# Kernel tuning notes

Hardware: AMD Instinct MI355X
Metric: run time of the kernel (lower is better)

Reference implementation:

```python
import jax, jax.numpy as jnp
import numpy as np
import math

BS, S, DIM, H = 2, 2048, 1024, 16
DH = DIM // H


def setup_inputs() -> dict:
    key = jax.random.key(0)
    ks = jax.random.split(key, 11)
    std = 1.0 / math.sqrt(DIM)
    inp = {
        "query": jax.random.normal(ks[0], (BS, S, DIM), jnp.float32),
        "key_": jax.random.normal(ks[1], (BS, S, DIM), jnp.float32),
        "value": jax.random.normal(ks[2], (BS, S, DIM), jnp.float32),
        "mask": jnp.ones((BS, S), jnp.int32),
        "q_w": jax.random.normal(ks[3], (DIM, DIM), jnp.float32) * std,
        "q_b": jnp.zeros((DIM,), jnp.float32),
        "k_w": jax.random.normal(ks[4], (DIM, DIM), jnp.float32) * std,
        "k_b": jnp.zeros((DIM,), jnp.float32),
        "v_w": jax.random.normal(ks[5], (DIM, DIM), jnp.float32) * std,
        "v_b": jnp.zeros((DIM,), jnp.float32),
        "o_w": jax.random.normal(ks[6], (DIM, DIM), jnp.float32) * std,
        "o_b": jnp.zeros((DIM,), jnp.float32),
    }
    return inp


def _shape(x):
    # (bs, s, dim) -> (bs, h, s, dh)
    return x.reshape(BS, -1, H, DH).transpose(0, 2, 1, 3)


def reference(query, key_, value, mask, q_w, q_b, k_w, k_b, v_w, v_b, o_w, o_b):
    # linear projections (torch Linear: x @ W.T + b)
    q = _shape(query @ q_w.T + q_b) / math.sqrt(DH)
    k = _shape(key_ @ k_w.T + k_b)
    v = _shape(value @ v_w.T + v_b)
    # scores: (bs, h, s, s)
    scores = jnp.einsum("bhqd,bhkd->bhqk", q, k)
    pad = (mask == 0)[:, None, None, :]  # (bs,1,1,k_len)
    scores = jnp.where(pad, -jnp.inf, scores)
    weights = jax.nn.softmax(scores, axis=-1)
    context = jnp.einsum("bhqk,bhkd->bhqd", weights, v)
    context = context.transpose(0, 2, 1, 3).reshape(BS, -1, DIM)
    return context @ o_w.T + o_b
```

## Files before the change

kernel.cpp:

```cpp
#include <hip/hip_runtime.h>
#include <hip/hip_bf16.h>

#define BSZ 2
#define SEQ 2048
#define DIMN 1024
#define NH 16
#define DH 64
#define LOG2E 1.4426950408889634f

typedef unsigned short ushort_t;
typedef __attribute__((ext_vector_type(8))) short short8;
typedef __attribute__((ext_vector_type(4))) float float4v;

__device__ __forceinline__ ushort_t f2bf(float f) {
    union { float f; unsigned int u; } c; c.f = f;
    return (ushort_t)((c.u + 0x8000u) >> 16);
}
__device__ __forceinline__ unsigned int pkbf(float a, float b) {
    __hip_bfloat162 h = __float22bfloat162_rn(make_float2(a, b));
    unsigned int u; __builtin_memcpy(&u, &h, 4); return u;
}
__device__ __forceinline__ unsigned int pkbf_asm(float a, float b) {
    unsigned int d;
    asm("v_cvt_pk_bf16_f32 %0, %1, %2" : "=v"(d) : "v"(a), "v"(b));
    return d;
}
__device__ __forceinline__ float exp2_raw(float x) {
    float d; asm("v_exp_f32 %0, %1" : "=v"(d) : "v"(x)); return d;
}
__device__ __forceinline__ float max3f(float a, float b, float c) {
    float d; asm("v_max3_f32 %0, %1, %2, %3" : "=v"(d) : "v"(a), "v"(b), "v"(c)); return d;
}
__device__ __forceinline__ void gld16(const ushort_t* g, ushort_t* l) {
    __builtin_amdgcn_global_load_lds(
        (const __attribute__((address_space(1))) unsigned int*)g,
        (__attribute__((address_space(3))) unsigned int*)l, 16, 0, 0);
}

__global__ __launch_bounds__(256) void cvt_all(
    const float* __restrict__ w0, const float* __restrict__ w1,
    const float* __restrict__ w2, const float* __restrict__ w3,
    const float* __restrict__ x0, const float* __restrict__ x1,
    const float* __restrict__ x2,
    ushort_t* __restrict__ o0, ushort_t* __restrict__ o1,
    ushort_t* __restrict__ o2, ushort_t* __restrict__ o3,
    ushort_t* __restrict__ xb)
{
    const int y = blockIdx.y;
    if (y < 4) {
        const float* s; ushort_t* d;
        switch (y) {
            case 0: s = w0; d = o0; break;
            case 1: s = w1; d = o1; break;
            case 2: s = w2; d = o2; break;
            default: s = w3; d = o3; break;
        }
        int i = (blockIdx.x * 256 + threadIdx.x) * 4;
        float4v v = *(const float4v*)(s + i);
        uint2 o; o.x = pkbf(v[0], v[1]); o.y = pkbf(v[2], v[3]);
        *(uint2*)(d + i) = o;
    } else {
        const int m = y - 4;
        const float* s = (m == 0) ? x0 : (m == 1) ? x1 : x2;
        ushort_t* d = xb + (size_t)m * (BSZ * SEQ * DIMN);
        size_t base = (size_t)blockIdx.x * 4096;
#pragma unroll
        for (int j = 0; j < 4; ++j) {
            size_t i = base + j * 1024 + threadIdx.x * 4;
            float4v v = *(const float4v*)(s + i);
            uint2 o; o.x = pkbf(v[0], v[1]); o.y = pkbf(v[2], v[3]);
            *(uint2*)(d + i) = o;
        }
    }
}

__global__ __launch_bounds__(256) void gemm_qkv(
    const float* __restrict__ xq, const float* __restrict__ xk, const float* __restrict__ xv,
    const ushort_t* __restrict__ Wq, const ushort_t* __restrict__ Wk, const ushort_t* __restrict__ Wv,
    const float* __restrict__ qb, const float* __restrict__ kb, const float* __restrict__ vb,
    ushort_t* __restrict__ Qp, ushort_t* __restrict__ Kp, ushort_t* __restrict__ VpT)
{
    __shared__ ushort_t As[128 * 72];
    __shared__ ushort_t Bs[128 * 72];
    const int tid  = threadIdx.x;
    const int lane = tid & 63;
    const int w    = tid >> 6;
    const int wm   = w >> 1, wn = w & 1;
    const int quad = lane >> 4;
    const int l16  = lane & 15;
    const int mBase = blockIdx.y * 128;
    const int nGlob = blockIdx.x * 128;
    const int z     = nGlob >> 10;
    const int nBase = nGlob & 1023;
    const float*    A    = (z == 0) ? xq : (z == 1) ? xk : xv;
    const ushort_t* W    = (z == 0) ? Wq : (z == 1) ? Wk : Wv;
    const float*    bias = (z == 0) ? qb : (z == 1) ? kb : vb;

    float4v acc[4][4];
    const float4v z4 = {0.f, 0.f, 0.f, 0.f};
#pragma unroll
    for (int i = 0; i < 4; ++i)
#pragma unroll
        for (int j = 0; j < 4; ++j) acc[i][j] = z4;

    for (int k0 = 0; k0 < 1024; k0 += 64) {
        float4v a[4][2];
        short8  wb[4];
#pragma unroll
        for (int it = 0; it < 4; ++it) {
            int c = it * 256 + tid, row = c >> 3, col = (c & 7) * 8;
            const float* g = A + (size_t)(mBase + row) * 1024 + k0 + col;
            a[it][0] = *(const float4v*)g;
            a[it][1] = *(const float4v*)(g + 4);
            wb[it] = *(const short8*)(W + (size_t)(nBase + row) * 1024 + k0 + col);
        }
        __syncthreads();
#pragma unroll
        for (int it = 0; it < 4; ++it) {
            int c = it * 256 + tid, row = c >> 3, col = (c & 7) * 8;
            uint4 ua;
            ua.x = pkbf(a[it][0][0], a[it][0][1]); ua.y = pkbf(a[it][0][2], a[it][0][3]);
            ua.z = pkbf(a[it][1][0], a[it][1][1]); ua.w = pkbf(a[it][1][2], a[it][1][3]);
            *(uint4*)&As[row * 72 + col] = ua;
            *(short8*)&Bs[row * 72 + col] = wb[it];
        }
        __syncthreads();

#pragma unroll
        for (int ksub = 0; ksub < 2; ++ksub) {
            short8 af[4], bf[4];
#pragma unroll
            for (int mt = 0; mt < 4; ++mt)
                af[mt] = *(const short8*)&As[(wm * 64 + mt * 16 + l16) * 72 + ksub * 32 + quad * 8];
#pragma unroll
            for (int nt = 0; nt < 4; ++nt)
                bf[nt] = *(const short8*)&Bs[(wn * 64 + nt * 16 + l16) * 72 + ksub * 32 + quad * 8];
#pragma unroll
            for (int mt = 0; mt < 4; ++mt)
#pragma unroll
                for (int nt = 0; nt < 4; ++nt)
                    acc[mt][nt] = __builtin_amdgcn_mfma_f32_16x16x32_bf16(af[mt], bf[nt], acc[mt][nt], 0, 0, 0);
        }
    }

    const float scale = (z == 0) ? 0.125f * LOG2E : 1.0f;
    if (z < 2) {
        ushort_t* C = (z == 0) ? Qp : Kp;
#pragma unroll
        for (int mt = 0; mt < 4; ++mt)
#pragma unroll
            for (int nt = 0; nt < 4; ++nt) {
                int colg = nBase + wn * 64 + nt * 16 + l16;
                float bv = bias[colg];
#pragma unroll
                for (int r = 0; r < 4; ++r) {
                    int rowg = mBase + wm * 64 + mt * 16 + quad * 4 + r;
                    C[(size_t)rowg * 1024 + colg] = f2bf((acc[mt][nt][r] + bv) * scale);
                }
            }
    } else {
#pragma unroll
        for (int mt = 0; mt < 4; ++mt)
#pragma unroll
            for (int nt = 0; nt < 4; ++nt) {
                int n = nBase + wn * 64 + nt * 16 + l16;
                int hh = n >> 6, d = n & 63;
                float bv = bias[n];
                int rowg = mBase + wm * 64 + mt * 16 + quad * 4;
                int b = rowg >> 11, s = rowg & 2047;
                uint2 pk;
                pk.x = pkbf(acc[mt][nt][0] + bv, acc[mt][nt][1] + bv);
                pk.y = pkbf(acc[mt][nt][2] + bv, acc[mt][nt][3] + bv);
                *(uint2*)&VpT[(((size_t)(b * 16 + hh) * 64 + d) << 11) + s] = pk;
            }
    }
}

__global__ __launch_bounds__(256) void gemm_qkv_fast(
    const ushort_t* __restrict__ Xb,
    const ushort_t* __restrict__ Wq, const ushort_t* __restrict__ Wk, const ushort_t* __restrict__ Wv,
    const float* __restrict__ qb, const float* __restrict__ kb, const float* __restrict__ vb,
    ushort_t* __restrict__ Qp, ushort_t* __restrict__ Kp, ushort_t* __restrict__ VpT)
{
    __shared__ __align__(16) ushort_t As[128 * 64];
    __shared__ __align__(16) ushort_t Bs[128 * 64];
    const int tid  = threadIdx.x;
    const int lane = tid & 63;
    const int w    = tid >> 6;
    const int wm   = w >> 1, wn = w & 1;
    const int quad = lane >> 4;
    const int l16  = lane & 15;
    const int sw   = l16 & 7;
    const int mBase = blockIdx.y * 128;
    const int nGlob = blockIdx.x * 128;
    const int z     = nGlob >> 10;
    const int nBase = nGlob & 1023;
    const ushort_t* A    = Xb + (size_t)z * (BSZ * SEQ * DIMN);
    const ushort_t* W    = (z == 0) ? Wq : (z == 1) ? Wk : Wv;
    const float*    bias = (z == 0) ? qb : (z == 1) ? kb : vb;

    const int srow = tid >> 3;
    const int sc   = tid & 7;

    float4v acc[4][4];
    const float4v z4 = {0.f, 0.f, 0.f, 0.f};
#pragma unroll
    for (int i = 0; i < 4; ++i)
#pragma unroll
        for (int j = 0; j < 4; ++j) acc[i][j] = z4;

    for (int k0 = 0; k0 < 1024; k0 += 64) {
#pragma unroll
        for (int itq = 0; itq < 4; ++itq) {
            int row = itq * 32 + srow;
            int colsw = (sc ^ (row & 7)) * 8;
            gld16(A + (size_t)(mBase + row) * 1024 + k0 + colsw, &As[(itq * 32 + w * 8) * 64]);
            gld16(W + (size_t)(nBase + row) * 1024 + k0 + colsw, &Bs[(itq * 32 + w * 8) * 64]);
        }
        __syncthreads();

#pragma unroll
        for (int ksub = 0; ksub < 2; ++ksub) {
            short8 af[4], bf[4];
#pragma unroll
            for (int mt = 0; mt < 4; ++mt)
                af[mt] = *(const short8*)&As[(wm * 64 + mt * 16 + l16) * 64 + ((ksub * 4 + quad) ^ sw) * 8];
#pragma unroll
            for (int nt = 0; nt < 4; ++nt)
                bf[nt] = *(const short8*)&Bs[(wn * 64 + nt * 16 + l16) * 64 + ((ksub * 4 + quad) ^ sw) * 8];
#pragma unroll
            for (int mt = 0; mt < 4; ++mt)
#pragma unroll
                for (int nt = 0; nt < 4; ++nt)
                    acc[mt][nt] = __builtin_amdgcn_mfma_f32_16x16x32_bf16(af[mt], bf[nt], acc[mt][nt], 0, 0, 0);
        }
        __syncthreads();
    }

    const float scale = (z == 0) ? 0.125f * LOG2E : 1.0f;
    if (z < 2) {
        ushort_t* C = (z == 0) ? Qp : Kp;
#pragma unroll
        for (int mt = 0; mt < 4; ++mt)
#pragma unroll
            for (int nt = 0; nt < 4; ++nt) {
                int colg = nBase + wn * 64 + nt * 16 + l16;
                float bv = bias[colg];
#pragma unroll
                for (int r = 0; r < 4; ++r) {
                    int rowg = mBase + wm * 64 + mt * 16 + quad * 4 + r;
                    C[(size_t)rowg * 1024 + colg] = f2bf((acc[mt][nt][r] + bv) * scale);
                }
            }
    } else {
#pragma unroll
        for (int mt = 0; mt < 4; ++mt)
#pragma unroll
            for (int nt = 0; nt < 4; ++nt) {
                int n = nBase + wn * 64 + nt * 16 + l16;
                int hh = n >> 6, d = n & 63;
                float bv = bias[n];
                int rowg = mBase + wm * 64 + mt * 16 + quad * 4;
                int b = rowg >> 11, s = rowg & 2047;
                uint2 pk;
                pk.x = pkbf(acc[mt][nt][0] + bv, acc[mt][nt][1] + bv);
                pk.y = pkbf(acc[mt][nt][2] + bv, acc[mt][nt][3] + bv);
                *(uint2*)&VpT[(((size_t)(b * 16 + hh) * 64 + d) << 11) + s] = pk;
            }
    }
}

__global__ __launch_bounds__(256) void gemm_o(
    const ushort_t* __restrict__ A, const ushort_t* __restrict__ W,
    const float* __restrict__ bias, float* __restrict__ C)
{
    __shared__ ushort_t As[128 * 72];
    __shared__ ushort_t Bs[64 * 72];
    const int tid  = threadIdx.x;
    const int lane = tid & 63;
    const int w    = tid >> 6;
    const int wm   = w & 1, wn = w >> 1;
    const int quad = lane >> 4;
    const int l16  = lane & 15;
    const int mBase = blockIdx.y * 128;
    const int nBase = blockIdx.x * 64;

    float4v acc[4][2];
    const float4v z4 = {0.f, 0.f, 0.f, 0.f};
#pragma unroll
    for (int mt = 0; mt < 4; ++mt)
#pragma unroll
        for (int nt = 0; nt < 2; ++nt) acc[mt][nt] = z4;

    for (int k0 = 0; k0 < 1024; k0 += 64) {
        short8 ab[4], wb[2];
#pragma unroll
        for (int it = 0; it < 4; ++it) {
            int c = it * 256 + tid, row = c >> 3, col = (c & 7) * 8;
            ab[it] = *(const short8*)(A + (size_t)(mBase + row) * 1024 + k0 + col);
        }
#pragma unroll
        for (int it = 0; it < 2; ++it) {
            int c = it * 256 + tid, row = c >> 3, col = (c & 7) * 8;
            wb[it] = *(const short8*)(W + (size_t)(nBase + row) * 1024 + k0 + col);
        }
        __syncthreads();
#pragma unroll
        for (int it = 0; it < 4; ++it) {
            int c = it * 256 + tid, row = c >> 3, col = (c & 7) * 8;
            *(short8*)&As[row * 72 + col] = ab[it];
        }
#pragma unroll
        for (int it = 0; it < 2; ++it) {
            int c = it * 256 + tid, row = c >> 3, col = (c & 7) * 8;
            *(short8*)&Bs[row * 72 + col] = wb[it];
        }
        __syncthreads();

#pragma unroll
        for (int ksub = 0; ksub < 2; ++ksub) {
            short8 af[4], bf[2];
#pragma unroll
            for (int mt = 0; mt < 4; ++mt)
                af[mt] = *(const short8*)&As[(wm * 64 + mt * 16 + l16) * 72 + ksub * 32 + quad * 8];
#pragma unroll
            for (int nt = 0; nt < 2; ++nt)
                bf[nt] = *(const short8*)&Bs[(wn * 32 + nt * 16 + l16) * 72 + ksub * 32 + quad * 8];
#pragma unroll
            for (int mt = 0; mt < 4; ++mt)
#pragma unroll
                for (int nt = 0; nt < 2; ++nt)
                    acc[mt][nt] = __builtin_amdgcn_mfma_f32_16x16x32_bf16(af[mt], bf[nt], acc[mt][nt], 0, 0, 0);
        }
    }

#pragma unroll
    for (int mt = 0; mt < 4; ++mt)
#pragma unroll
        for (int nt = 0; nt < 2; ++nt) {
            int colg = nBase + wn * 32 + nt * 16 + l16;
            float bv = bias[colg];
#pragma unroll
            for (int r = 0; r < 4; ++r) {
                int rowg = mBase + wm * 64 + mt * 16 + quad * 4 + r;
                C[(size_t)rowg * 1024 + colg] = acc[mt][nt][r] + bv;
            }
        }
}

__global__ __launch_bounds__(512) void attn_kernel(
    const ushort_t* __restrict__ Qp, const ushort_t* __restrict__ Kp,
    const ushort_t* __restrict__ VpT, const int* __restrict__ mask,
    ushort_t* __restrict__ Cp)
{
    __shared__ __align__(16) ushort_t Qs[128 * 64];
    __shared__ __align__(16) ushort_t Ks[2][64 * 64];
    __shared__ __align__(16) ushort_t Vt[2][64 * 64];
    __shared__ int s_mok[8];

    const int tid  = threadIdx.x;
    const int lane = tid & 63;
    const int w    = tid >> 6;
    const int quad = lane >> 4;
    const int l16  = lane & 15;
    const int sw   = l16 & 7;
    const int b    = blockIdx.x >> 4;
    const int h    = blockIdx.x & 15;
    const int q0   = blockIdx.y * 128;

    const int srow = tid >> 3;
    const int sc   = tid & 7;
    const int gsc  = (sc ^ (srow & 7)) * 8;
    const ushort_t* Vbase = VpT + ((size_t)(b * 16 + h) * 64) * 2048;
    const ushort_t* Kbase = Kp + (size_t)b * SEQ * DIMN + h * DH;
    const ushort_t* Qbase = Qp + (size_t)(b * SEQ + q0) * DIMN + h * DH;

    {
        int m0 = mask[b * SEQ + tid];
        int m1 = mask[b * SEQ + 512 + tid];
        int m2 = mask[b * SEQ + 1024 + tid];
        int m3 = mask[b * SEQ + 1536 + tid];
        int ok = __all((m0 != 0) & (m1 != 0) & (m2 != 0) & (m3 != 0));
        if (lane == 0) s_mok[w] = ok;
    }

#pragma unroll
    for (int it2 = 0; it2 < 2; ++it2) {
        int row = it2 * 64 + srow;
        gld16(Qbase + (size_t)row * DIMN + ((sc ^ (row & 7)) * 8),
              &Qs[(it2 * 64 + w * 8) * 64]);
    }
    gld16(Kbase + (size_t)srow * DIMN + gsc, &Ks[0][w * 512]);
    gld16(Vbase + (size_t)srow * 2048 + gsc, &Vt[0][w * 512]);
    __syncthreads();

    const int mall = s_mok[0] & s_mok[1] & s_mok[2] & s_mok[3]
                   & s_mok[4] & s_mok[5] & s_mok[6] & s_mok[7];

    short8 bq[2];
#pragma unroll
    for (int ks = 0; ks < 2; ++ks)
        bq[ks] = *(const short8*)&Qs[(w * 16 + l16) * 64 + ((4 * ks + quad) ^ sw) * 8];

    const float4v z4 = {0.f, 0.f, 0.f, 0.f};
    float4v Oacc[4];
#pragma unroll
    for (int vt = 0; vt < 4; ++vt) Oacc[vt] = z4;
    float4v Lacc = z4;
    float mrow = 0.0f;
    float4v mneg4 = z4;

    short8 ones;
#pragma unroll
    for (int j = 0; j < 8; ++j) ones[j] = (short)0x3F80;

    const int NT = SEQ / 64;
#pragma unroll 2
    for (int it = 0; it < NT; ++it) {
        const int bsel = it & 1;
        const int kt0  = it * 64;

        if (it + 1 < NT) {
            int kn = kt0 + 64;
            gld16(Kbase + (size_t)(kn + srow) * DIMN + gsc, &Ks[bsel ^ 1][w * 512]);
            gld16(Vbase + (size_t)srow * 2048 + kn + gsc, &Vt[bsel ^ 1][w * 512]);
        }

        float4v Sv[4];
        __builtin_amdgcn_s_setprio(1);
#pragma unroll
        for (int kt = 0; kt < 4; ++kt) {
            short8 ak = *(const short8*)&Ks[bsel][(kt * 16 + l16) * 64 + (quad ^ sw) * 8];
            Sv[kt] = __builtin_amdgcn_mfma_f32_16x16x32_bf16(ak, bq[0], mneg4, 0, 0, 0);
        }
#pragma unroll
        for (int kt = 0; kt < 4; ++kt) {
            short8 ak = *(const short8*)&Ks[bsel][(kt * 16 + l16) * 64 + ((4 + quad) ^ sw) * 8];
            Sv[kt] = __builtin_amdgcn_mfma_f32_16x16x32_bf16(ak, bq[1], Sv[kt], 0, 0, 0);
        }
        __builtin_amdgcn_s_setprio(0);

        if (!mall) {
            int4 mv4[4];
#pragma unroll
            for (int kt = 0; kt < 4; ++kt)
                mv4[kt] = *(const int4*)(mask + b * SEQ + kt0 + kt * 16 + quad * 4);
#pragma unroll
            for (int kt = 0; kt < 4; ++kt) {
                int4 mv = mv4[kt];
#pragma unroll
                for (int r = 0; r < 4; ++r) {
                    int m = (r == 0) ? mv.x : (r == 1) ? mv.y : (r == 2) ? mv.z : mv.w;
                    Sv[kt][r] += (m == 0) ? -1e30f : 0.0f;
                }
            }
        }

        float a0 = max3f(Sv[0][0], Sv[0][1], Sv[0][2]);
        float a1 = max3f(Sv[0][3], Sv[1][0], Sv[1][1]);
        float a2 = max3f(Sv[1][2], Sv[1][3], Sv[2][0]);
        float a3 = max3f(Sv[2][1], Sv[2][2], Sv[2][3]);
        float a4 = max3f(Sv[3][0], Sv[3][1], Sv[3][2]);
        float b0 = max3f(a0, a1, Sv[3][3]);
        float b1 = max3f(a2, a3, a4);
        float mx = fmaxf(b0, b1);
        mx = fmaxf(mx, __shfl_xor(mx, 16));
        mx = fmaxf(mx, __shfl_xor(mx, 32));
        if (!__all(mx <= 8.0f)) {
            float d = fmaxf(mx, 0.0f);
            float alpha = exp2_raw(-d);
            mrow += d;
#pragma unroll
            for (int vt = 0; vt < 4; ++vt) Oacc[vt] *= alpha;
            Lacc *= alpha;
#pragma unroll
            for (int kt = 0; kt < 4; ++kt)
#pragma unroll
                for (int r = 0; r < 4; ++r) Sv[kt][r] -= d;
            mneg4[0] = -mrow; mneg4[1] = -mrow; mneg4[2] = -mrow; mneg4[3] = -mrow;
        }
#pragma unroll
        for (int kt = 0; kt < 4; ++kt)
#pragma unroll
            for (int r = 0; r < 4; ++r) Sv[kt][r] = exp2_raw(Sv[kt][r]);

#pragma unroll
        for (int kt = 0; kt < 4; ++kt) {
            uint2 pk;
            pk.x = pkbf_asm(Sv[kt][0], Sv[kt][1]);
            pk.y = pkbf_asm(Sv[kt][2], Sv[kt][3]);
            int chunk = (2 * kt + (quad >> 1)) ^ sw;
            *(uint2*)&Qs[(w * 16 + l16) * 64 + chunk * 8 + (quad & 1) * 4] = pk;
        }

        __builtin_amdgcn_s_setprio(1);
#pragma unroll
        for (int ks = 0; ks < 2; ++ks) {
            short8 bp = *(const short8*)&Qs[(w * 16 + l16) * 64 + ((4 * ks + quad) ^ sw) * 8];
            Lacc = __builtin_amdgcn_mfma_f32_16x16x32_bf16(ones, bp, Lacc, 0, 0, 0);
#pragma unroll
            for (int vt = 0; vt < 4; ++vt) {
                short8 av = *(const short8*)&Vt[bsel][(vt * 16 + l16) * 64 + ((4 * ks + quad) ^ sw) * 8];
                Oacc[vt] = __builtin_amdgcn_mfma_f32_16x16x32_bf16(av, bp, Oacc[vt], 0, 0, 0);
            }
        }
        __builtin_amdgcn_s_setprio(0);

        __syncthreads();
    }

    float inv = 1.0f / Lacc[0];
    int row = q0 + w * 16 + l16;
#pragma unroll
    for (int vt = 0; vt < 4; ++vt) {
        uint2 pk;
        pk.x = pkbf_asm(Oacc[vt][0] * inv, Oacc[vt][1] * inv);
        pk.y = pkbf_asm(Oacc[vt][2] * inv, Oacc[vt][3] * inv);
        *(uint2*)&Cp[(size_t)(b * SEQ + row) * DIMN + h * DH + vt * 16 + quad * 4] = pk;
    }
}

extern "C" void kernel_launch(void* const* d_in, const int* in_sizes, int n_in,
                              void* d_out, int out_size, void* d_ws, size_t ws_size,
                              hipStream_t stream) {
    const float* x_q = (const float*)d_in[0];
    const float* x_k = (const float*)d_in[1];
    const float* x_v = (const float*)d_in[2];
    const int*   msk = (const int*)d_in[3];
    const float* q_w = (const float*)d_in[4];
    const float* q_b = (const float*)d_in[5];
    const float* k_w = (const float*)d_in[6];
    const float* k_b = (const float*)d_in[7];
    const float* v_w = (const float*)d_in[8];
    const float* v_b = (const float*)d_in[9];
    const float* o_w = (const float*)d_in[10];
    const float* o_b = (const float*)d_in[11];
    float* out = (float*)d_out;

    const size_t NEL = (size_t)BSZ * SEQ * DIMN;
    const size_t WEL = (size_t)DIMN * DIMN;
    ushort_t* Qp  = (ushort_t*)d_ws;
    ushort_t* Kp  = Qp + NEL;
    ushort_t* VpT = Kp + NEL;
    ushort_t* Wq  = VpT + NEL;
    ushort_t* Wk  = Wq + WEL;
    ushort_t* Wv  = Wk + WEL;
    ushort_t* Wo  = Wv + WEL;
    ushort_t* Xb  = Wo + WEL;
    ushort_t* Cp  = Qp;

    const bool fast = ws_size >= ((size_t)56 << 20);
    if (fast) {
        cvt_all<<<dim3(1024, 7), 256, 0, stream>>>(q_w, k_w, v_w, o_w, x_q, x_k, x_v,
                                                   Wq, Wk, Wv, Wo, Xb);
        gemm_qkv_fast<<<dim3(24, 32), 256, 0, stream>>>(Xb, Wq, Wk, Wv,
                                                        q_b, k_b, v_b, Qp, Kp, VpT);
    } else {
        cvt_all<<<dim3(1024, 4), 256, 0, stream>>>(q_w, k_w, v_w, o_w, x_q, x_k, x_v,
                                                   Wq, Wk, Wv, Wo, Xb);
        gemm_qkv<<<dim3(24, 32), 256, 0, stream>>>(x_q, x_k, x_v, Wq, Wk, Wv,
                                                   q_b, k_b, v_b, Qp, Kp, VpT);
    }
    attn_kernel<<<dim3(BSZ * NH, SEQ / 128), 512, 0, stream>>>(Qp, Kp, VpT, msk, Cp);
    gemm_o<<<dim3(16, 32), 256, 0, stream>>>(Cp, Wo, o_b, out);
}
```

Baseline: 227.4 us.

## Software-pipeline attention PV with next QK; use async swizzled loads in output GEMM

The attention loop is restructured so iteration t computes QK^T scores for tile t while doing the P·V MFMAs for tile t-1. P is double-buffered and V triple-buffered, which lets the matrix work overlap the softmax exp/max math within a wave. The output-projection GEMM swaps its register-staged global-to-LDS copy with padded rows for direct gld16 loads into an XOR-swizzled unpadded LDS layout. This removes the register staging and padding, at the cost of an extra barrier per k-step. The attention change adds LDS usage and register pressure from the prologue and epilogue.

```diff
diff --git a/kernel.cpp b/kernel.cpp
--- a/kernel.cpp
+++ b/kernel.cpp
@@ -274,16 +274,19 @@
     const ushort_t* __restrict__ A, const ushort_t* __restrict__ W,
     const float* __restrict__ bias, float* __restrict__ C)
 {
-    __shared__ ushort_t As[128 * 72];
-    __shared__ ushort_t Bs[64 * 72];
+    __shared__ __align__(16) ushort_t As[128 * 64];
+    __shared__ __align__(16) ushort_t Bs[64 * 64];
     const int tid  = threadIdx.x;
     const int lane = tid & 63;
     const int w    = tid >> 6;
     const int wm   = w & 1, wn = w >> 1;
     const int quad = lane >> 4;
     const int l16  = lane & 15;
+    const int sw   = l16 & 7;
     const int mBase = blockIdx.y * 128;
     const int nBase = blockIdx.x * 64;
+    const int srow = tid >> 3;
+    const int sc   = tid & 7;
 
     float4v acc[4][2];
     const float4v z4 = {0.f, 0.f, 0.f, 0.f};
@@ -293,27 +296,17 @@
         for (int nt = 0; nt < 2; ++nt) acc[mt][nt] = z4;
 
     for (int k0 = 0; k0 < 1024; k0 += 64) {
-        short8 ab[4], wb[2];
-#pragma unroll
-        for (int it = 0; it < 4; ++it) {
-            int c = it * 256 + tid, row = c >> 3, col = (c & 7) * 8;
-            ab[it] = *(const short8*)(A + (size_t)(mBase + row) * 1024 + k0 + col);
-        }
-#pragma unroll
-        for (int it = 0; it < 2; ++it) {
-            int c = it * 256 + tid, row = c >> 3, col = (c & 7) * 8;
-            wb[it] = *(const short8*)(W + (size_t)(nBase + row) * 1024 + k0 + col);
-        }
-        __syncthreads();
-#pragma unroll
-        for (int it = 0; it < 4; ++it) {
-            int c = it * 256 + tid, row = c >> 3, col = (c & 7) * 8;
-            *(short8*)&As[row * 72 + col] = ab[it];
-        }
-#pragma unroll
-        for (int it = 0; it < 2; ++it) {
-            int c = it * 256 + tid, row = c >> 3, col = (c & 7) * 8;
-            *(short8*)&Bs[row * 72 + col] = wb[it];
+#pragma unroll
+        for (int itq = 0; itq < 4; ++itq) {
+            int row = itq * 32 + srow;
+            gld16(A + (size_t)(mBase + row) * 1024 + k0 + ((sc ^ (row & 7)) * 8),
+                  &As[(itq * 32 + w * 8) * 64]);
+        }
+#pragma unroll
+        for (int itq = 0; itq < 2; ++itq) {
+            int row = itq * 32 + srow;
+            gld16(W + (size_t)(nBase + row) * 1024 + k0 + ((sc ^ (row & 7)) * 8),
+                  &Bs[(itq * 32 + w * 8) * 64]);
         }
         __syncthreads();
 
@@ -322,16 +315,17 @@
             short8 af[4], bf[2];
 #pragma unroll
             for (int mt = 0; mt < 4; ++mt)
-                af[mt] = *(const short8*)&As[(wm * 64 + mt * 16 + l16) * 72 + ksub * 32 + quad * 8];
+                af[mt] = *(const short8*)&As[(wm * 64 + mt * 16 + l16) * 64 + ((ksub * 4 + quad) ^ sw) * 8];
 #pragma unroll
             for (int nt = 0; nt < 2; ++nt)
-                bf[nt] = *(const short8*)&Bs[(wn * 32 + nt * 16 + l16) * 72 + ksub * 32 + quad * 8];
+                bf[nt] = *(const short8*)&Bs[(wn * 32 + nt * 16 + l16) * 64 + ((ksub * 4 + quad) ^ sw) * 8];
 #pragma unroll
             for (int mt = 0; mt < 4; ++mt)
 #pragma unroll
                 for (int nt = 0; nt < 2; ++nt)
                     acc[mt][nt] = __builtin_amdgcn_mfma_f32_16x16x32_bf16(af[mt], bf[nt], acc[mt][nt], 0, 0, 0);
         }
+        __syncthreads();
     }
 
 #pragma unroll
@@ -353,9 +347,9 @@
     const ushort_t* __restrict__ VpT, const int* __restrict__ mask,
     ushort_t* __restrict__ Cp)
 {
-    __shared__ __align__(16) ushort_t Qs[128 * 64];
+    __shared__ __align__(16) ushort_t Ps[2][128 * 64];
     __shared__ __align__(16) ushort_t Ks[2][64 * 64];
-    __shared__ __align__(16) ushort_t Vt[2][64 * 64];
+    __shared__ __align__(16) ushort_t Vt[3][64 * 64];
     __shared__ int s_mok[8];
 
     const int tid  = threadIdx.x;
@@ -388,7 +382,7 @@
     for (int it2 = 0; it2 < 2; ++it2) {
         int row = it2 * 64 + srow;
         gld16(Qbase + (size_t)row * DIMN + ((sc ^ (row & 7)) * 8),
-              &Qs[(it2 * 64 + w * 8) * 64]);
+              &Ps[0][(it2 * 64 + w * 8) * 64]);
     }
     gld16(Kbase + (size_t)srow * DIMN + gsc, &Ks[0][w * 512]);
     gld16(Vbase + (size_t)srow * 2048 + gsc, &Vt[0][w * 512]);
@@ -400,7 +394,7 @@
     short8 bq[2];
 #pragma unroll
     for (int ks = 0; ks < 2; ++ks)
-        bq[ks] = *(const short8*)&Qs[(w * 16 + l16) * 64 + ((4 * ks + quad) ^ sw) * 8];
+        bq[ks] = *(const short8*)&Ps[0][(w * 16 + l16) * 64 + ((4 * ks + quad) ^ sw) * 8];
 
     const float4v z4 = {0.f, 0.f, 0.f, 0.f};
     float4v Oacc[4];
@@ -415,39 +409,30 @@
     for (int j = 0; j < 8; ++j) ones[j] = (short)0x3F80;
 
     const int NT = SEQ / 64;
-#pragma unroll 2
-    for (int it = 0; it < NT; ++it) {
-        const int bsel = it & 1;
-        const int kt0  = it * 64;
-
-        if (it + 1 < NT) {
-            int kn = kt0 + 64;
-            gld16(Kbase + (size_t)(kn + srow) * DIMN + gsc, &Ks[bsel ^ 1][w * 512]);
-            gld16(Vbase + (size_t)srow * 2048 + kn + gsc, &Vt[bsel ^ 1][w * 512]);
-        }
+    const int prow = (w * 16 + l16) * 64;
+
+    {
+        gld16(Kbase + (size_t)(64 + srow) * DIMN + gsc, &Ks[1][w * 512]);
+        gld16(Vbase + (size_t)srow * 2048 + 64 + gsc, &Vt[1][w * 512]);
 
         float4v Sv[4];
         __builtin_amdgcn_s_setprio(1);
 #pragma unroll
         for (int kt = 0; kt < 4; ++kt) {
-            short8 ak = *(const short8*)&Ks[bsel][(kt * 16 + l16) * 64 + (quad ^ sw) * 8];
+            short8 ak = *(const short8*)&Ks[0][(kt * 16 + l16) * 64 + (quad ^ sw) * 8];
             Sv[kt] = __builtin_amdgcn_mfma_f32_16x16x32_bf16(ak, bq[0], mneg4, 0, 0, 0);
         }
 #pragma unroll
         for (int kt = 0; kt < 4; ++kt) {
-            short8 ak = *(const short8*)&Ks[bsel][(kt * 16 + l16) * 64 + ((4 + quad) ^ sw) * 8];
+            short8 ak = *(const short8*)&Ks[0][(kt * 16 + l16) * 64 + ((4 + quad) ^ sw) * 8];
             Sv[kt] = __builtin_amdgcn_mfma_f32_16x16x32_bf16(ak, bq[1], Sv[kt], 0, 0, 0);
         }
         __builtin_amdgcn_s_setprio(0);
 
         if (!mall) {
-            int4 mv4[4];
-#pragma unroll
-            for (int kt = 0; kt < 4; ++kt)
-                mv4[kt] = *(const int4*)(mask + b * SEQ + kt0 + kt * 16 + quad * 4);
 #pragma unroll
             for (int kt = 0; kt < 4; ++kt) {
-                int4 mv = mv4[kt];
+                int4 mv = *(const int4*)(mask + b * SEQ + kt * 16 + quad * 4);
 #pragma unroll
                 for (int r = 0; r < 4; ++r) {
                     int m = (r == 0) ? mv.x : (r == 1) ? mv.y : (r == 2) ? mv.z : mv.w;
@@ -490,23 +475,111 @@
             pk.x = pkbf_asm(Sv[kt][0], Sv[kt][1]);
             pk.y = pkbf_asm(Sv[kt][2], Sv[kt][3]);
             int chunk = (2 * kt + (quad >> 1)) ^ sw;
-            *(uint2*)&Qs[(w * 16 + l16) * 64 + chunk * 8 + (quad & 1) * 4] = pk;
-        }
-
+            *(uint2*)&Ps[0][prow + chunk * 8 + (quad & 1) * 4] = pk;
+        }
+        __syncthreads();
+    }
+
+    ushort_t* vRd  = Vt[0];
+    ushort_t* vCur = Vt[1];
+    ushort_t* vWr  = Vt[2];
+
+#pragma unroll 2
+    for (int t = 1; t < NT; ++t) {
+        const int kt0 = t * 64;
+
+        if (t + 1 < NT) {
+            gld16(Kbase + (size_t)(kt0 + 64 + srow) * DIMN + gsc, &Ks[(t + 1) & 1][w * 512]);
+            gld16(Vbase + (size_t)srow * 2048 + kt0 + 64 + gsc, vWr + w * 512);
+        }
+
+        float4v Sv[4];
         __builtin_amdgcn_s_setprio(1);
 #pragma unroll
+        for (int kt = 0; kt < 4; ++kt) {
+            short8 ak = *(const short8*)&Ks[t & 1][(kt * 16 + l16) * 64 + (quad ^ sw) * 8];
+            Sv[kt] = __builtin_amdgcn_mfma_f32_16x16x32_bf16(ak, bq[0], mneg4, 0, 0, 0);
+        }
+#pragma unroll
+        for (int kt = 0; kt < 4; ++kt) {
+            short8 ak = *(const short8*)&Ks[t & 1][(kt * 16 + l16) * 64 + ((4 + quad) ^ sw) * 8];
+            Sv[kt] = __builtin_amdgcn_mfma_f32_16x16x32_bf16(ak, bq[1], Sv[kt], 0, 0, 0);
+        }
+#pragma unroll
         for (int ks = 0; ks < 2; ++ks) {
-            short8 bp = *(const short8*)&Qs[(w * 16 + l16) * 64 + ((4 * ks + quad) ^ sw) * 8];
+            short8 bp = *(const short8*)&Ps[(t - 1) & 1][prow + ((4 * ks + quad) ^ sw) * 8];
             Lacc = __builtin_amdgcn_mfma_f32_16x16x32_bf16(ones, bp, Lacc, 0, 0, 0);
 #pragma unroll
             for (int vt = 0; vt < 4; ++vt) {
-                short8 av = *(const short8*)&Vt[bsel][(vt * 16 + l16) * 64 + ((4 * ks + quad) ^ sw) * 8];
+                short8 av = *(const short8*)(vRd + (vt * 16 + l16) * 64 + ((4 * ks + quad) ^ sw) * 8);
                 Oacc[vt] = __builtin_amdgcn_mfma_f32_16x16x32_bf16(av, bp, Oacc[vt], 0, 0, 0);
             }
         }
         __builtin_amdgcn_s_setprio(0);
 
-        __syncthreads();
+        if (!mall) {
+#pragma unroll
+            for (int kt = 0; kt < 4; ++kt) {
+                int4 mv = *(const int4*)(mask + b * SEQ + kt0 + kt * 16 + quad * 4);
+#pragma unroll
+                for (int r = 0; r < 4; ++r) {
+                    int m = (r == 0) ? mv.x : (r == 1) ? mv.y : (r == 2) ? mv.z : mv.w;
+                    Sv[kt][r] += (m == 0) ? -1e30f : 0.0f;
+                }
+            }
+        }
+
+        float a0 = max3f(Sv[0][0], Sv[0][1], Sv[0][2]);
+        float a1 = max3f(Sv[0][3], Sv[1][0], Sv[1][1]);
+        float a2 = max3f(Sv[1][2], Sv[1][3], Sv[2][0]);
+        float a3 = max3f(Sv[2][1], Sv[2][2], Sv[2][3]);
+        float a4 = max3f(Sv[3][0], Sv[3][1], Sv[3][2]);
+        float b0 = max3f(a0, a1, Sv[3][3]);
+        float b1 = max3f(a2, a3, a4);
+        float mx = fmaxf(b0, b1);
+        mx = fmaxf(mx, __shfl_xor(mx, 16));
+        mx = fmaxf(mx, __shfl_xor(mx, 32));
+        if (!__all(mx <= 8.0f)) {
+            float d = fmaxf(mx, 0.0f);
+            float alpha = exp2_raw(-d);
+            mrow += d;
+#pragma unroll
+            for (int vt = 0; vt < 4; ++vt) Oacc[vt] *= alpha;
+            Lacc *= alpha;
+#pragma unroll
+            for (int kt = 0; kt < 4; ++kt)
+#pragma unroll
+                for (int r = 0; r < 4; ++r) Sv[kt][r] -= d;
+            mneg4[0] = -mrow; mneg4[1] = -mrow; mneg4[2] = -mrow; mneg4[3] = -mrow;
+        }
+#pragma unroll
+        for (int kt = 0; kt < 4; ++kt)
+#pragma unroll
+            for (int r = 0; r < 4; ++r) Sv[kt][r] = exp2_raw(Sv[kt][r]);
+
+#pragma unroll
+        for (int kt = 0; kt < 4; ++kt) {
+            uint2 pk;
+            pk.x = pkbf_asm(Sv[kt][0], Sv[kt][1]);
+            pk.y = pkbf_asm(Sv[kt][2], Sv[kt][3]);
+            int chunk = (2 * kt + (quad >> 1)) ^ sw;
+            *(uint2*)&Ps[t & 1][prow + chunk * 8 + (quad & 1) * 4] = pk;
+        }
+
+        __syncthreads();
+
+        ushort_t* tmp = vRd; vRd = vCur; vCur = vWr; vWr = tmp;
+    }
+
+#pragma unroll
+    for (int ks = 0; ks < 2; ++ks) {
+        short8 bp = *(const short8*)&Ps[(NT - 1) & 1][prow + ((4 * ks + quad) ^ sw) * 8];
+        Lacc = __builtin_amdgcn_mfma_f32_16x16x32_bf16(ones, bp, Lacc, 0, 0, 0);
+#pragma unroll
+        for (int vt = 0; vt < 4; ++vt) {
+            short8 av = *(const short8*)(vRd + (vt * 16 + l16) * 64 + ((4 * ks + quad) ^ sw) * 8);
+            Oacc[vt] = __builtin_amdgcn_mfma_f32_16x16x32_bf16(av, bp, Oacc[vt], 0, 0, 0);
+        }
     }
 
     float inv = 1.0f / Lacc[0];
```

Result: no change. 225.3 us (-0.9%).

## Halve attention query tile and use direct-to-LDS swizzled loads in output GEMM

Applied to the files above, without the earlier changes.

The attention kernel drops from 128 to 64 query rows per block with 256 threads, doubling the grid. The aim is more blocks for occupancy and load balance, at the cost of twice the K/V tile reloads per query. The mask check now runs per wave with vectorized loads instead of through shared memory, and the row-max shuffles run only on the rescale path. The output GEMM now uses swizzled direct global-to-LDS loads instead of staging through registers into padded shared memory, which adds a trailing barrier.

```diff
diff --git a/kernel.cpp b/kernel.cpp
--- a/kernel.cpp
+++ b/kernel.cpp
@@ -274,16 +274,19 @@
     const ushort_t* __restrict__ A, const ushort_t* __restrict__ W,
     const float* __restrict__ bias, float* __restrict__ C)
 {
-    __shared__ ushort_t As[128 * 72];
-    __shared__ ushort_t Bs[64 * 72];
+    __shared__ __align__(16) ushort_t As[128 * 64];
+    __shared__ __align__(16) ushort_t Bs[64 * 64];
     const int tid  = threadIdx.x;
     const int lane = tid & 63;
     const int w    = tid >> 6;
     const int wm   = w & 1, wn = w >> 1;
     const int quad = lane >> 4;
     const int l16  = lane & 15;
+    const int sw   = l16 & 7;
     const int mBase = blockIdx.y * 128;
     const int nBase = blockIdx.x * 64;
+    const int srow = tid >> 3;
+    const int sc   = tid & 7;
 
     float4v acc[4][2];
     const float4v z4 = {0.f, 0.f, 0.f, 0.f};
@@ -293,27 +296,17 @@
         for (int nt = 0; nt < 2; ++nt) acc[mt][nt] = z4;
 
     for (int k0 = 0; k0 < 1024; k0 += 64) {
-        short8 ab[4], wb[2];
-#pragma unroll
-        for (int it = 0; it < 4; ++it) {
-            int c = it * 256 + tid, row = c >> 3, col = (c & 7) * 8;
-            ab[it] = *(const short8*)(A + (size_t)(mBase + row) * 1024 + k0 + col);
-        }
-#pragma unroll
-        for (int it = 0; it < 2; ++it) {
-            int c = it * 256 + tid, row = c >> 3, col = (c & 7) * 8;
-            wb[it] = *(const short8*)(W + (size_t)(nBase + row) * 1024 + k0 + col);
-        }
-        __syncthreads();
-#pragma unroll
-        for (int it = 0; it < 4; ++it) {
-            int c = it * 256 + tid, row = c >> 3, col = (c & 7) * 8;
-            *(short8*)&As[row * 72 + col] = ab[it];
-        }
-#pragma unroll
-        for (int it = 0; it < 2; ++it) {
-            int c = it * 256 + tid, row = c >> 3, col = (c & 7) * 8;
-            *(short8*)&Bs[row * 72 + col] = wb[it];
+#pragma unroll
+        for (int itq = 0; itq < 4; ++itq) {
+            int row = itq * 32 + srow;
+            gld16(A + (size_t)(mBase + row) * 1024 + k0 + ((sc ^ (row & 7)) * 8),
+                  &As[(itq * 32 + w * 8) * 64]);
+        }
+#pragma unroll
+        for (int itq = 0; itq < 2; ++itq) {
+            int row = itq * 32 + srow;
+            gld16(W + (size_t)(nBase + row) * 1024 + k0 + ((sc ^ (row & 7)) * 8),
+                  &Bs[(itq * 32 + w * 8) * 64]);
         }
         __syncthreads();
 
@@ -322,16 +315,17 @@
             short8 af[4], bf[2];
 #pragma unroll
             for (int mt = 0; mt < 4; ++mt)
-                af[mt] = *(const short8*)&As[(wm * 64 + mt * 16 + l16) * 72 + ksub * 32 + quad * 8];
+                af[mt] = *(const short8*)&As[(wm * 64 + mt * 16 + l16) * 64 + ((ksub * 4 + quad) ^ sw) * 8];
 #pragma unroll
             for (int nt = 0; nt < 2; ++nt)
-                bf[nt] = *(const short8*)&Bs[(wn * 32 + nt * 16 + l16) * 72 + ksub * 32 + quad * 8];
+                bf[nt] = *(const short8*)&Bs[(wn * 32 + nt * 16 + l16) * 64 + ((ksub * 4 + quad) ^ sw) * 8];
 #pragma unroll
             for (int mt = 0; mt < 4; ++mt)
 #pragma unroll
                 for (int nt = 0; nt < 2; ++nt)
                     acc[mt][nt] = __builtin_amdgcn_mfma_f32_16x16x32_bf16(af[mt], bf[nt], acc[mt][nt], 0, 0, 0);
         }
+        __syncthreads();
     }
 
 #pragma unroll
@@ -348,15 +342,14 @@
         }
 }
 
-__global__ __launch_bounds__(512) void attn_kernel(
+__global__ __launch_bounds__(256) void attn_kernel(
     const ushort_t* __restrict__ Qp, const ushort_t* __restrict__ Kp,
     const ushort_t* __restrict__ VpT, const int* __restrict__ mask,
     ushort_t* __restrict__ Cp)
 {
-    __shared__ __align__(16) ushort_t Qs[128 * 64];
+    __shared__ __align__(16) ushort_t Ps[64 * 64];
     __shared__ __align__(16) ushort_t Ks[2][64 * 64];
     __shared__ __align__(16) ushort_t Vt[2][64 * 64];
-    __shared__ int s_mok[8];
 
     const int tid  = threadIdx.x;
     const int lane = tid & 63;
@@ -366,41 +359,39 @@
     const int sw   = l16 & 7;
     const int b    = blockIdx.x >> 4;
     const int h    = blockIdx.x & 15;
-    const int q0   = blockIdx.y * 128;
-
-    const int srow = tid >> 3;
-    const int sc   = tid & 7;
-    const int gsc  = (sc ^ (srow & 7)) * 8;
+    const int q0   = blockIdx.y * 64;
+
+    const int srow8 = lane >> 3;
+    const int sc    = lane & 7;
+    const int gsc   = (sc ^ srow8) * 8;
     const ushort_t* Vbase = VpT + ((size_t)(b * 16 + h) * 64) * 2048;
     const ushort_t* Kbase = Kp + (size_t)b * SEQ * DIMN + h * DH;
     const ushort_t* Qbase = Qp + (size_t)(b * SEQ + q0) * DIMN + h * DH;
 
+    int mall;
     {
-        int m0 = mask[b * SEQ + tid];
-        int m1 = mask[b * SEQ + 512 + tid];
-        int m2 = mask[b * SEQ + 1024 + tid];
-        int m3 = mask[b * SEQ + 1536 + tid];
-        int ok = __all((m0 != 0) & (m1 != 0) & (m2 != 0) & (m3 != 0));
-        if (lane == 0) s_mok[w] = ok;
-    }
-
-#pragma unroll
-    for (int it2 = 0; it2 < 2; ++it2) {
-        int row = it2 * 64 + srow;
-        gld16(Qbase + (size_t)row * DIMN + ((sc ^ (row & 7)) * 8),
-              &Qs[(it2 * 64 + w * 8) * 64]);
-    }
-    gld16(Kbase + (size_t)srow * DIMN + gsc, &Ks[0][w * 512]);
-    gld16(Vbase + (size_t)srow * 2048 + gsc, &Vt[0][w * 512]);
+        int ok = 1;
+#pragma unroll
+        for (int j = 0; j < 8; ++j) {
+            int4 mv = *(const int4*)(mask + b * SEQ + j * 256 + lane * 4);
+            ok &= (mv.x != 0) & (mv.y != 0) & (mv.z != 0) & (mv.w != 0);
+        }
+        mall = __all(ok);
+    }
+
+#pragma unroll
+    for (int r = 0; r < 2; ++r) {
+        int row = r * 32 + w * 8 + srow8;
+        gld16(Qbase + (size_t)row * DIMN + gsc, &Ps[(r * 32 + w * 8) * 64]);
+        gld16(Kbase + (size_t)row * DIMN + gsc, &Ks[0][(r * 32 + w * 8) * 64]);
+        gld16(Vbase + (size_t)row * 2048 + gsc, &Vt[0][(r * 32 + w * 8) * 64]);
+    }
     __syncthreads();
 
-    const int mall = s_mok[0] & s_mok[1] & s_mok[2] & s_mok[3]
-                   & s_mok[4] & s_mok[5] & s_mok[6] & s_mok[7];
-
     short8 bq[2];
 #pragma unroll
     for (int ks = 0; ks < 2; ++ks)
-        bq[ks] = *(const short8*)&Qs[(w * 16 + l16) * 64 + ((4 * ks + quad) ^ sw) * 8];
+        bq[ks] = *(const short8*)&Ps[(w * 16 + l16) * 64 + ((4 * ks + quad) ^ sw) * 8];
 
     const float4v z4 = {0.f, 0.f, 0.f, 0.f};
     float4v Oacc[4];
@@ -415,39 +406,39 @@
     for (int j = 0; j < 8; ++j) ones[j] = (short)0x3F80;
 
     const int NT = SEQ / 64;
+    const int prow = (w * 16 + l16) * 64;
+
 #pragma unroll 2
-    for (int it = 0; it < NT; ++it) {
-        const int bsel = it & 1;
-        const int kt0  = it * 64;
-
-        if (it + 1 < NT) {
-            int kn = kt0 + 64;
-            gld16(Kbase + (size_t)(kn + srow) * DIMN + gsc, &Ks[bsel ^ 1][w * 512]);
-            gld16(Vbase + (size_t)srow * 2048 + kn + gsc, &Vt[bsel ^ 1][w * 512]);
+    for (int t = 0; t < NT; ++t) {
+        const int kt0 = t * 64;
+
+        if (t + 1 < NT) {
+#pragma unroll
+            for (int r = 0; r < 2; ++r) {
+                int row = r * 32 + w * 8 + srow8;
+                gld16(Kbase + (size_t)(kt0 + 64 + row) * DIMN + gsc, &Ks[(t + 1) & 1][(r * 32 + w * 8) * 64]);
+                gld16(Vbase + (size_t)row * 2048 + kt0 + 64 + gsc, &Vt[(t + 1) & 1][(r * 32 + w * 8) * 64]);
+            }
         }
 
         float4v Sv[4];
         __builtin_amdgcn_s_setprio(1);
 #pragma unroll
         for (int kt = 0; kt < 4; ++kt) {
-            short8 ak = *(const short8*)&Ks[bsel][(kt * 16 + l16) * 64 + (quad ^ sw) * 8];
+            short8 ak = *(const short8*)&Ks[t & 1][(kt * 16 + l16) * 64 + (quad ^ sw) * 8];
             Sv[kt] = __builtin_amdgcn_mfma_f32_16x16x32_bf16(ak, bq[0], mneg4, 0, 0, 0);
         }
 #pragma unroll
         for (int kt = 0; kt < 4; ++kt) {
-            short8 ak = *(const short8*)&Ks[bsel][(kt * 16 + l16) * 64 + ((4 + quad) ^ sw) * 8];
+            short8 ak = *(const short8*)&Ks[t & 1][(kt * 16 + l16) * 64 + ((4 + quad) ^ sw) * 8];
             Sv[kt] = __builtin_amdgcn_mfma_f32_16x16x32_bf16(ak, bq[1], Sv[kt], 0, 0, 0);
         }
         __builtin_amdgcn_s_setprio(0);
 
         if (!mall) {
-            int4 mv4[4];
-#pragma unroll
-            for (int kt = 0; kt < 4; ++kt)
-                mv4[kt] = *(const int4*)(mask + b * SEQ + kt0 + kt * 16 + quad * 4);
 #pragma unroll
             for (int kt = 0; kt < 4; ++kt) {
-                int4 mv = mv4[kt];
+                int4 mv = *(const int4*)(mask + b * SEQ + kt0 + kt * 16 + quad * 4);
 #pragma unroll
                 for (int r = 0; r < 4; ++r) {
                     int m = (r == 0) ? mv.x : (r == 1) ? mv.y : (r == 2) ? mv.z : mv.w;
@@ -464,10 +455,10 @@
         float b0 = max3f(a0, a1, Sv[3][3]);
         float b1 = max3f(a2, a3, a4);
         float mx = fmaxf(b0, b1);
-        mx = fmaxf(mx, __shfl_xor(mx, 16));
-        mx = fmaxf(mx, __shfl_xor(mx, 32));
         if (!__all(mx <= 8.0f)) {
-            float d = fmaxf(mx, 0.0f);
+            float m2 = fmaxf(mx, __shfl_xor(mx, 16));
+            m2 = fmaxf(m2, __shfl_xor(m2, 32));
+            float d = fmaxf(m2, 0.0f);
             float alpha = exp2_raw(-d);
             mrow += d;
 #pragma unroll
@@ -489,18 +480,18 @@
             uint2 pk;
             pk.x = pkbf_asm(Sv[kt][0], Sv[kt][1]);
             pk.y = pkbf_asm(Sv[kt][2], Sv[kt][3]);
-            int chunk = (2 * kt + (quad >> 1)) ^ sw;
-            *(uint2*)&Qs[(w * 16 + l16) * 64 + chunk * 8 + (quad & 1) * 4] = pk;
+            int chunk = ((2 * kt + (quad >> 1)) ^ sw) * 8 + (quad & 1) * 4;
+            *(uint2*)&Ps[prow + chunk] = pk;
         }
 
         __builtin_amdgcn_s_setprio(1);
 #pragma unroll
         for (int ks = 0; ks < 2; ++ks) {
-            short8 bp = *(const short8*)&Qs[(w * 16 + l16) * 64 + ((4 * ks + quad) ^ sw) * 8];
+            short8 bp = *(const short8*)&Ps[prow + ((4 * ks + quad) ^ sw) * 8];
             Lacc = __builtin_amdgcn_mfma_f32_16x16x32_bf16(ones, bp, Lacc, 0, 0, 0);
 #pragma unroll
             for (int vt = 0; vt < 4; ++vt) {
-                short8 av = *(const short8*)&Vt[bsel][(vt * 16 + l16) * 64 + ((4 * ks + quad) ^ sw) * 8];
+                short8 av = *(const short8*)&Vt[t & 1][(vt * 16 + l16) * 64 + ((4 * ks + quad) ^ sw) * 8];
                 Oacc[vt] = __builtin_amdgcn_mfma_f32_16x16x32_bf16(av, bp, Oacc[vt], 0, 0, 0);
             }
         }
@@ -561,6 +552,6 @@
         gemm_qkv<<<dim3(24, 32), 256, 0, stream>>>(x_q, x_k, x_v, Wq, Wk, Wv,
                                                    q_b, k_b, v_b, Qp, Kp, VpT);
     }
-    attn_kernel<<<dim3(BSZ * NH, SEQ / 128), 512, 0, stream>>>(Qp, Kp, VpT, msk, Cp);
+    attn_kernel<<<dim3(BSZ * NH, SEQ / 64), 256, 0, stream>>>(Qp, Kp, VpT, msk, Cp);
     gemm_o<<<dim3(16, 32), 256, 0, stream>>>(Cp, Wo, o_b, out);
 }
```

Result: slower. 253.0 us (+11.3%).
